# Performance work log

Measured on AMD Instinct MI355X. Metric: run time of the kernel, lower is better.

The kernel has to match this reference:

```python
import jax, jax.numpy as jnp
import numpy as np

N_NODES = 100000
N_EDGES = 800000
N_GRAPHS = 64
D_IN = 128
D_HID = 128
D_OUT = 128
N_VARS = 8


def setup_inputs() -> dict:
    key = jax.random.key(0)
    ks = jax.random.split(key, 12)
    s = 1.0 / np.sqrt(D_IN)
    inp = {
        "features": jax.random.normal(ks[0], (N_NODES, D_IN), jnp.float32),
        "src": jax.random.randint(ks[1], (N_EDGES,), 0, N_NODES, jnp.int32),
        "dst": jax.random.randint(ks[2], (N_EDGES,), 0, N_NODES, jnp.int32),
        "graph_id": jnp.sort(jax.random.randint(ks[3], (N_NODES,), 0, N_GRAPHS, jnp.int32)),
        # GINConv MLP params (Linear + ReLU per layer)
        "W1": jax.random.normal(ks[4], (D_IN, D_HID), jnp.float32) * s,
        "b1": jnp.zeros((D_HID,), jnp.float32),
        "W2": jax.random.normal(ks[5], (D_HID, D_HID), jnp.float32) * s,
        "b2": jnp.zeros((D_HID,), jnp.float32),
        "W3": jax.random.normal(ks[6], (D_HID, D_OUT), jnp.float32) * s,
        "b3": jnp.zeros((D_OUT,), jnp.float32),
        # final prediction head
        "Wp": jax.random.normal(ks[7], (D_OUT, N_VARS), jnp.float32) * s,
        "bp": jnp.zeros((N_VARS,), jnp.float32),
    }
    return inp


def reference(features, src, dst, graph_id, W1, b1, W2, b2, W3, b3, Wp, bp):
    N = features.shape[0]

    def gin_layer(x, W, b):
        # DGL GINConv with eps=0: apply_func(x + sum_{j in N(i)} x_j)
        agg = jax.ops.segment_sum(x[src], dst, num_segments=N)  # [N, d]
        return jax.nn.relu((x + agg) @ W + b)

    h = gin_layer(features, W1, b1)  # dropout p=0 -> identity
    h = gin_layer(h, W2, b2)
    h = gin_layer(h, W3, b3)

    # dgl.mean_nodes: ragged per-graph mean readout
    sums = jax.ops.segment_sum(h, graph_id, num_segments=N_GRAPHS)          # [G, d]
    cnts = jax.ops.segment_sum(jnp.ones((N, 1), h.dtype), graph_id, num_segments=N_GRAPHS)
    pooled = sums / jnp.maximum(cnts, 1.0)
    return pooled @ Wp + bp  # [G, n_vars]
```

## Files before the change

### kernel.cpp

```cpp
#include <hip/hip_runtime.h>
#include <cstddef>

#define NN 100000
#define NE 800000
#define NG 64
#define DD 128
#define NV 8
#define NS 8
#define SCAN_CH 1024
#define SCAN_NB ((NN + SCAN_CH - 1) / SCAN_CH)
#define NPC 256
#define NCHUNK ((NN + NPC - 1) / NPC)

#define CVT_BLKS 6250
#define WT_BLKS 192
#define HIST_BLKS 3125
#define HCH 392
#define ECH ((NE + HCH - 1) / HCH)
#define RNG 12500

typedef __attribute__((ext_vector_type(8))) short bf16x8;
typedef __attribute__((ext_vector_type(4))) float f32x4;
typedef __attribute__((ext_vector_type(2))) unsigned int u32x2;

__device__ inline float lo2f(unsigned int u) {
  union { unsigned int i; float f; } x;
  x.i = u << 16;
  return x.f;
}
__device__ inline float hi2f(unsigned int u) {
  union { unsigned int i; float f; } x;
  x.i = u & 0xffff0000u;
  return x.f;
}
__device__ inline unsigned int pk2(float a, float b) {
  unsigned int r;
  asm("v_cvt_pk_bf16_f32 %0, %1, %2" : "=v"(r) : "v"(a), "v"(b));
  return r;
}
__device__ inline unsigned short f2b(float f) {
  union { float f; unsigned int i; } x;
  x.f = f;
  unsigned int r = x.i + 0x7fffu + ((x.i >> 16) & 1u);
  return (unsigned short)(r >> 16);
}

__global__ __launch_bounds__(256) void prep(const float* __restrict__ feat,
                                            const float* __restrict__ W1,
                                            const float* __restrict__ W2,
                                            const float* __restrict__ W3,
                                            unsigned short* __restrict__ xs,
                                            unsigned short* __restrict__ Wt) {
  int b = blockIdx.x;
  if (b < CVT_BLKS) {
    int tid = b * 256 + threadIdx.x;
    int l = tid & 63, w = tid >> 6;
    int s = w & 7, nb = w >> 3;
    int node = nb * 32 + (l >> 1);
    int half = l & 1;
    const float* p = feat + (size_t)node * DD + s * 16 + half * 8;
    float4 v0 = *(const float4*)p;
    float4 v1 = *(const float4*)(p + 4);
    uint4 o;
    o.x = pk2(v0.x, v0.y);
    o.y = pk2(v0.z, v0.w);
    o.z = pk2(v1.x, v1.y);
    o.w = pk2(v1.z, v1.w);
    *(uint4*)((char*)xs + ((size_t)s * NN + node) * 32 + half * 16) = o;
  } else {
    int idx = (b - CVT_BLKS) * 256 + threadIdx.x;
    int w = idx >> 14, r = idx & 16383;
    const float* W = (w == 0) ? W1 : (w == 1) ? W2 : W3;
    Wt[idx] = f2b(W[(r & 127) * DD + (r >> 7)]);
  }
}

__global__ __launch_bounds__(256) void hist_dst(const int* __restrict__ dst,
                                                int* __restrict__ deg) {
  int e = blockIdx.x * 256 + threadIdx.x;
  if (e < NE) atomicAdd(&deg[dst[e]], 1);
}

__global__ __launch_bounds__(256) void scan1(const int* __restrict__ deg,
                                             int* __restrict__ excl,
                                             int* __restrict__ bsum) {
  __shared__ int ts[256];
  int base = blockIdx.x * SCAN_CH;
  int t = threadIdx.x;
  int v[4];
  int s = 0;
#pragma unroll
  for (int i = 0; i < 4; i++) {
    int idx = base + t * 4 + i;
    v[i] = (idx < NN) ? deg[idx] : 0;
    s += v[i];
  }
  ts[t] = s;
  __syncthreads();
  for (int off = 1; off < 256; off <<= 1) {
    int val = (t >= off) ? ts[t - off] : 0;
    __syncthreads();
    ts[t] += val;
    __syncthreads();
  }
  if (t == 255) bsum[blockIdx.x] = ts[255];
  int run = ts[t] - s;
#pragma unroll
  for (int i = 0; i < 4; i++) {
    int idx = base + t * 4 + i;
    if (idx < NN) excl[idx] = run;
    run += v[i];
  }
}

__global__ __launch_bounds__(128) void scan2(int* __restrict__ bsum, int nb) {
  __shared__ int sh[128];
  int t = threadIdx.x;
  int v = (t < nb) ? bsum[t] : 0;
  sh[t] = v;
  __syncthreads();
  for (int off = 1; off < 128; off <<= 1) {
    int u = (t >= off) ? sh[t - off] : 0;
    __syncthreads();
    sh[t] += u;
    __syncthreads();
  }
  if (t < nb) bsum[t] = sh[t] - v;
}

__global__ __launch_bounds__(256) void scan3(int* __restrict__ rowp,
                                             const int* __restrict__ bsum,
                                             int* __restrict__ cursor) {
  int i = blockIdx.x * blockDim.x + threadIdx.x;
  if (i < NN) {
    int v = rowp[i] + bsum[i / SCAN_CH];
    rowp[i] = v;
    cursor[i] = v;
  }
  if (i == 0) rowp[NN] = NE;
}

__global__ __launch_bounds__(256) void fill_csr(const int* __restrict__ src,
                                                const int* __restrict__ dst,
                                                int* __restrict__ cursor,
                                                int* __restrict__ csrb) {
  int r = blockIdx.x & 7, chunk = blockIdx.x >> 3;
  int lo = r * RNG, hi = lo + RNG;
  int e0 = chunk * ECH;
  int e1 = e0 + ECH;
  if (e1 > NE) e1 = NE;
  for (int e = e0 + threadIdx.x; e < e1; e += 256) {
    int d = dst[e];
    if (d >= lo && d < hi) {
      int pos = atomicAdd(&cursor[d], 1);
      csrb[pos] = src[e] << 5;
    }
  }
}

__global__ __launch_bounds__(256) void gather_slice(const unsigned short* __restrict__ xs,
                                                    const int* __restrict__ csrb,
                                                    const int* __restrict__ rowp,
                                                    unsigned short* __restrict__ aggs) {
  const int s = blockIdx.x & 7;
  const int chunk = blockIdx.x >> 3;
  const char* __restrict__ xsl = (const char*)xs + (size_t)s * NN * 32;
  char* __restrict__ asl = (char*)aggs + (size_t)s * NN * 32;
  const int li = threadIdx.x & 3;
  const int grp = threadIdx.x >> 2;
  const int node0 = chunk * NPC;
  int node1 = node0 + NPC;
  if (node1 > NN) node1 = NN;
  const int lo8 = li * 8;
  for (int n = node0 + grp; n < node1; n += 64) {
    int beg = rowp[n], end = rowp[n + 1];
    u32x2 sv = *(const u32x2*)(xsl + (size_t)n * 32 + lo8);
    float a0 = lo2f(sv.x), a1 = hi2f(sv.x), a2 = lo2f(sv.y), a3 = hi2f(sv.y);
    float c0 = 0.f, c1 = 0.f, c2 = 0.f, c3 = 0.f;
    int e = beg;
    int off = (beg < end) ? csrb[(beg + li < end) ? beg + li : end - 1] : 0;
    for (; e + 4 <= end; e += 4) {
      int ne = e + 4;
      int off_next = 0;
      if (ne < end) off_next = csrb[(ne + li < end) ? ne + li : end - 1];
      int o0 = __shfl(off, 0, 4);
      int o1 = __shfl(off, 1, 4);
      int o2 = __shfl(off, 2, 4);
      int o3 = __shfl(off, 3, 4);
      u32x2 v0 = *(const u32x2*)(xsl + (unsigned int)o0 + lo8);
      u32x2 v1 = *(const u32x2*)(xsl + (unsigned int)o1 + lo8);
      u32x2 v2 = *(const u32x2*)(xsl + (unsigned int)o2 + lo8);
      u32x2 v3 = *(const u32x2*)(xsl + (unsigned int)o3 + lo8);
      a0 += lo2f(v0.x); a1 += hi2f(v0.x); a2 += lo2f(v0.y); a3 += hi2f(v0.y);
      c0 += lo2f(v1.x); c1 += hi2f(v1.x); c2 += lo2f(v1.y); c3 += hi2f(v1.y);
      a0 += lo2f(v2.x); a1 += hi2f(v2.x); a2 += lo2f(v2.y); a3 += hi2f(v2.y);
      c0 += lo2f(v3.x); c1 += hi2f(v3.x); c2 += lo2f(v3.y); c3 += hi2f(v3.y);
      off = off_next;
    }
    if (e < end) {
      int rem = end - e;
      for (int j = 0; j < rem; j++) {
        int oj = __shfl(off, j, 4);
        u32x2 v = *(const u32x2*)(xsl + (unsigned int)oj + lo8);
        a0 += lo2f(v.x); a1 += hi2f(v.x); a2 += lo2f(v.y); a3 += hi2f(v.y);
      }
    }
    u32x2 o;
    o.x = pk2(a0 + c0, a1 + c1);
    o.y = pk2(a2 + c2, a3 + c3);
    *(u32x2*)(asl + (size_t)n * 32 + lo8) = o;
  }
}

template <int POOL>
__global__ __launch_bounds__(256) void gemm_mfma(const unsigned short* __restrict__ A,
                                                 const unsigned short* __restrict__ Wt,
                                                 const float* __restrict__ bias,
                                                 unsigned short* __restrict__ H,
                                                 const int* __restrict__ gid,
                                                 float* __restrict__ sums,
                                                 float* __restrict__ cnts) {
  __shared__ uint4 a_sh4[1024];
  __shared__ uint4 w_sh4[2048];
  __shared__ int gsh[64];
  char* a_sh = (char*)a_sh4;
  char* w_sh = (char*)w_sh4;
  const int t = threadIdx.x;
  const int block_row = blockIdx.x * 64;

  if (POOL) {
    if (t < 64) gsh[t] = (block_row + t < NN) ? gid[block_row + t] : -1;
  }

#pragma unroll
  for (int p = 0; p < 8; p++) {
    int lin = p * 4096 + t * 16;
    int row = lin >> 8, inner = lin & 255;
    uint4 v = *(const uint4*)((const char*)Wt + lin);
    *(uint4*)(w_sh + row * 256 + (inner ^ ((row & 7) << 4))) = v;
  }
#pragma unroll
  for (int p = 0; p < 4; p++) {
    int lin = p * 4096 + t * 16;
    int row = lin >> 8, inner = lin & 255;
    int grow = block_row + row;
    uint4 v = make_uint4(0u, 0u, 0u, 0u);
    if (grow < NN) {
      int slice = inner >> 5, half = (inner >> 4) & 1;
      v = *(const uint4*)((const char*)A + ((size_t)slice * NN + grow) * 32 + half * 16);
    }
    *(uint4*)(a_sh + row * 256 + (inner ^ ((row & 7) << 4))) = v;
  }
  __syncthreads();

  const int wid = t >> 6, lane = t & 63;
  const int rowbase = wid * 16;
  const int lr = lane & 15, lk = lane >> 4;

  f32x4 acc[8];
#pragma unroll
  for (int i = 0; i < 8; i++) acc[i] = (f32x4){0.f, 0.f, 0.f, 0.f};

#pragma unroll
  for (int c = 0; c < 4; c++) {
    int arow = rowbase + lr;
    bf16x8 af = *(const bf16x8*)(a_sh + arow * 256 + ((c * 64 + lk * 16) ^ ((arow & 7) << 4)));
#pragma unroll
    for (int nt = 0; nt < 8; nt++) {
      int bcol = nt * 16 + lr;
      bf16x8 bf = *(const bf16x8*)(w_sh + bcol * 256 + ((c * 64 + lk * 16) ^ ((bcol & 7) << 4)));
      acc[nt] = __builtin_amdgcn_mfma_f32_16x16x32_bf16(af, bf, acc[nt], 0, 0, 0);
    }
  }
  __syncthreads();

  float* osh = (float*)w_sh;
#pragma unroll
  for (int nt = 0; nt < 8; nt++) {
    int col = nt * 16 + lr;
    float bv = bias[col];
#pragma unroll
    for (int r = 0; r < 4; r++) {
      int row = rowbase + lk * 4 + r;
      osh[row * 128 + col] = fmaxf(acc[nt][r] + bv, 0.f);
    }
  }
  __syncthreads();

  if (POOL == 0) {
#pragma unroll
    for (int i = 0; i < 8; i++) {
      int fidx = i * 1024 + t * 4;
      float4 v = *(const float4*)(osh + fidx);
      int row = fidx >> 7, col = fidx & 127;
      int grow = block_row + row;
      if (grow < NN) {
        int slice = col >> 4, w = col & 15;
        u32x2 o;
        o.x = pk2(v.x, v.y);
        o.y = pk2(v.z, v.w);
        *(u32x2*)(H + ((size_t)slice * NN + grow) * 16 + w) = o;
      }
    }
  } else {
    if (t < 128) {
      int f = t;
      float acc2 = 0.f;
      int cnt = 0;
      int cur = gsh[0];
      for (int r = 0; r < 64; r++) {
        int g = gsh[r];
        if (g < 0) break;
        if (g != cur) {
          unsafeAtomicAdd(&sums[cur * DD + f], acc2);
          if (f == 0) unsafeAtomicAdd(&cnts[cur], (float)cnt);
          acc2 = 0.f;
          cnt = 0;
          cur = g;
        }
        acc2 += osh[r * 128 + f];
        cnt++;
      }
      if (cur >= 0 && cnt > 0) {
        unsafeAtomicAdd(&sums[cur * DD + f], acc2);
        if (f == 0) unsafeAtomicAdd(&cnts[cur], (float)cnt);
      }
    }
  }
}

__global__ __launch_bounds__(512) void head(const float* __restrict__ sums,
                                            const float* __restrict__ cnts,
                                            const float* __restrict__ Wp,
                                            const float* __restrict__ bp,
                                            float* __restrict__ out) {
  int t = threadIdx.x;
  int g = t >> 3;
  int v = t & 7;
  float cnt = cnts[g];
  if (cnt < 1.f) cnt = 1.f;
  float acc = 0.f;
  for (int d = 0; d < DD; d++) acc += sums[g * DD + d] * Wp[d * NV + v];
  out[t] = acc / cnt + bp[v];
}

extern "C" void kernel_launch(void* const* d_in, const int* in_sizes, int n_in,
                              void* d_out, int out_size, void* d_ws, size_t ws_size,
                              hipStream_t stream) {
  const float* feat = (const float*)d_in[0];
  const int* src = (const int*)d_in[1];
  const int* dst = (const int*)d_in[2];
  const int* gid = (const int*)d_in[3];
  const float* W1 = (const float*)d_in[4];
  const float* b1 = (const float*)d_in[5];
  const float* W2 = (const float*)d_in[6];
  const float* b2 = (const float*)d_in[7];
  const float* W3 = (const float*)d_in[8];
  const float* b3 = (const float*)d_in[9];
  const float* Wp = (const float*)d_in[10];
  const float* bp = (const float*)d_in[11];
  float* out = (float*)d_out;

  char* ws = (char*)d_ws;
  const size_t matb = (size_t)NN * DD;
  unsigned short* xs0 = (unsigned short*)ws;
  unsigned short* hs = xs0 + matb;
  unsigned short* aggs = hs + matb;
  unsigned short* wtb = aggs + matb;
  float* sums = (float*)(wtb + 3 * DD * DD);
  float* cnts = sums + NG * DD;
  int* deg = (int*)(cnts + NG);
  int* rowp = deg + NN;
  int* cursor = rowp + NN + 1;
  int* bsum = cursor + NN;
  int* csrb = bsum + 128;

  const int nzero = NG * DD + NG + NN;
  hipMemsetAsync(sums, 0, (size_t)nzero * 4, stream);

  prep<<<CVT_BLKS + WT_BLKS, 256, 0, stream>>>(feat, W1, W2, W3, xs0, wtb);
  hist_dst<<<HIST_BLKS, 256, 0, stream>>>(dst, deg);

  scan1<<<SCAN_NB, 256, 0, stream>>>(deg, rowp, bsum);
  scan2<<<1, 128, 0, stream>>>(bsum, SCAN_NB);
  scan3<<<(NN + 255) / 256, 256, 0, stream>>>(rowp, bsum, cursor);
  fill_csr<<<8 * HCH, 256, 0, stream>>>(src, dst, cursor, csrb);

  const int ggrid = NCHUNK * NS;
  const int mgrid = (NN + 63) / 64;
  gather_slice<<<ggrid, 256, 0, stream>>>(xs0, csrb, rowp, aggs);
  gemm_mfma<0><<<mgrid, 256, 0, stream>>>(aggs, wtb, b1, hs, nullptr, nullptr, nullptr);
  gather_slice<<<ggrid, 256, 0, stream>>>(hs, csrb, rowp, aggs);
  gemm_mfma<0><<<mgrid, 256, 0, stream>>>(aggs, wtb + DD * DD, b2, xs0, nullptr, nullptr, nullptr);
  gather_slice<<<ggrid, 256, 0, stream>>>(xs0, csrb, rowp, aggs);
  gemm_mfma<1><<<mgrid, 256, 0, stream>>>(aggs, wtb + 2 * DD * DD, b3, nullptr, gid, sums, cnts);

  head<<<1, 512, 0, stream>>>(sums, cnts, Wp, bp, out);
}
```

Measured before the change: 308.0 us.

## Widen feature slices from 32B to 64B per node in gather layout

Changes the sliced bf16 feature layout from 8 slices of 16 features (32B rows) to 4 slices of 32 features (64B rows). The gather kernel now uses 8 lanes per node and unrolls 8 edges per step, and each block handles half a chunk for one slice. Prep, fill_csr offset shift, gemm load and gemm store are updated to match. The aim is fewer, wider random gathers per edge with better cache-line use, at the cost of a larger per-slice working set in cache.

```diff
diff --git a/kernel.cpp b/kernel.cpp
--- a/kernel.cpp
+++ b/kernel.cpp
@@ -6,7 +6,6 @@
 #define NG 64
 #define DD 128
 #define NV 8
-#define NS 8
 #define SCAN_CH 1024
 #define SCAN_NB ((NN + SCAN_CH - 1) / SCAN_CH)
 #define NPC 256
@@ -54,11 +53,8 @@
   int b = blockIdx.x;
   if (b < CVT_BLKS) {
     int tid = b * 256 + threadIdx.x;
-    int l = tid & 63, w = tid >> 6;
-    int s = w & 7, nb = w >> 3;
-    int node = nb * 32 + (l >> 1);
-    int half = l & 1;
-    const float* p = feat + (size_t)node * DD + s * 16 + half * 8;
+    int n = tid >> 4, part = tid & 15;
+    const float* p = feat + (size_t)n * DD + part * 8;
     float4 v0 = *(const float4*)p;
     float4 v1 = *(const float4*)(p + 4);
     uint4 o;
@@ -66,7 +62,8 @@
     o.y = pk2(v0.z, v0.w);
     o.z = pk2(v1.x, v1.y);
     o.w = pk2(v1.z, v1.w);
-    *(uint4*)((char*)xs + ((size_t)s * NN + node) * 32 + half * 16) = o;
+    int s2 = part >> 2, sub = part & 3;
+    *(uint4*)((char*)xs + ((size_t)s2 * NN + n) * 64 + sub * 16) = o;
   } else {
     int idx = (b - CVT_BLKS) * 256 + threadIdx.x;
     int w = idx >> 14, r = idx & 16383;
@@ -153,7 +150,7 @@
     int d = dst[e];
     if (d >= lo && d < hi) {
       int pos = atomicAdd(&cursor[d], 1);
-      csrb[pos] = src[e] << 5;
+      csrb[pos] = src[e] << 6;
     }
   }
 }
@@ -162,45 +159,58 @@
                                                     const int* __restrict__ csrb,
                                                     const int* __restrict__ rowp,
                                                     unsigned short* __restrict__ aggs) {
-  const int s = blockIdx.x & 7;
+  const int q = blockIdx.x & 7;
+  const int s2 = q & 3, half = q >> 2;
   const int chunk = blockIdx.x >> 3;
-  const char* __restrict__ xsl = (const char*)xs + (size_t)s * NN * 32;
-  char* __restrict__ asl = (char*)aggs + (size_t)s * NN * 32;
-  const int li = threadIdx.x & 3;
-  const int grp = threadIdx.x >> 2;
-  const int node0 = chunk * NPC;
-  int node1 = node0 + NPC;
+  const char* __restrict__ xsl = (const char*)xs + (size_t)s2 * NN * 64;
+  char* __restrict__ asl = (char*)aggs + (size_t)s2 * NN * 64;
+  const int li = threadIdx.x & 7;
+  const int grp = threadIdx.x >> 3;
+  int node0 = chunk * NPC + half * (NPC / 2);
+  int node1 = node0 + NPC / 2;
   if (node1 > NN) node1 = NN;
   const int lo8 = li * 8;
-  for (int n = node0 + grp; n < node1; n += 64) {
+  for (int n = node0 + grp; n < node1; n += 32) {
     int beg = rowp[n], end = rowp[n + 1];
-    u32x2 sv = *(const u32x2*)(xsl + (size_t)n * 32 + lo8);
+    u32x2 sv = *(const u32x2*)(xsl + (size_t)n * 64 + lo8);
     float a0 = lo2f(sv.x), a1 = hi2f(sv.x), a2 = lo2f(sv.y), a3 = hi2f(sv.y);
     float c0 = 0.f, c1 = 0.f, c2 = 0.f, c3 = 0.f;
     int e = beg;
     int off = (beg < end) ? csrb[(beg + li < end) ? beg + li : end - 1] : 0;
-    for (; e + 4 <= end; e += 4) {
-      int ne = e + 4;
+    for (; e + 8 <= end; e += 8) {
+      int ne = e + 8;
       int off_next = 0;
       if (ne < end) off_next = csrb[(ne + li < end) ? ne + li : end - 1];
-      int o0 = __shfl(off, 0, 4);
-      int o1 = __shfl(off, 1, 4);
-      int o2 = __shfl(off, 2, 4);
-      int o3 = __shfl(off, 3, 4);
+      int o0 = __shfl(off, 0, 8);
+      int o1 = __shfl(off, 1, 8);
+      int o2 = __shfl(off, 2, 8);
+      int o3 = __shfl(off, 3, 8);
+      int o4 = __shfl(off, 4, 8);
+      int o5 = __shfl(off, 5, 8);
+      int o6 = __shfl(off, 6, 8);
+      int o7 = __shfl(off, 7, 8);
       u32x2 v0 = *(const u32x2*)(xsl + (unsigned int)o0 + lo8);
       u32x2 v1 = *(const u32x2*)(xsl + (unsigned int)o1 + lo8);
       u32x2 v2 = *(const u32x2*)(xsl + (unsigned int)o2 + lo8);
       u32x2 v3 = *(const u32x2*)(xsl + (unsigned int)o3 + lo8);
+      u32x2 v4 = *(const u32x2*)(xsl + (unsigned int)o4 + lo8);
+      u32x2 v5 = *(const u32x2*)(xsl + (unsigned int)o5 + lo8);
+      u32x2 v6 = *(const u32x2*)(xsl + (unsigned int)o6 + lo8);
+      u32x2 v7 = *(const u32x2*)(xsl + (unsigned int)o7 + lo8);
       a0 += lo2f(v0.x); a1 += hi2f(v0.x); a2 += lo2f(v0.y); a3 += hi2f(v0.y);
       c0 += lo2f(v1.x); c1 += hi2f(v1.x); c2 += lo2f(v1.y); c3 += hi2f(v1.y);
       a0 += lo2f(v2.x); a1 += hi2f(v2.x); a2 += lo2f(v2.y); a3 += hi2f(v2.y);
       c0 += lo2f(v3.x); c1 += hi2f(v3.x); c2 += lo2f(v3.y); c3 += hi2f(v3.y);
+      a0 += lo2f(v4.x); a1 += hi2f(v4.x); a2 += lo2f(v4.y); a3 += hi2f(v4.y);
+      c0 += lo2f(v5.x); c1 += hi2f(v5.x); c2 += lo2f(v5.y); c3 += hi2f(v5.y);
+      a0 += lo2f(v6.x); a1 += hi2f(v6.x); a2 += lo2f(v6.y); a3 += hi2f(v6.y);
+      c0 += lo2f(v7.x); c1 += hi2f(v7.x); c2 += lo2f(v7.y); c3 += hi2f(v7.y);
       off = off_next;
     }
     if (e < end) {
       int rem = end - e;
       for (int j = 0; j < rem; j++) {
-        int oj = __shfl(off, j, 4);
+        int oj = __shfl(off, j, 8);
         u32x2 v = *(const u32x2*)(xsl + (unsigned int)oj + lo8);
         a0 += lo2f(v.x); a1 += hi2f(v.x); a2 += lo2f(v.y); a3 += hi2f(v.y);
       }
@@ -208,7 +218,7 @@
     u32x2 o;
     o.x = pk2(a0 + c0, a1 + c1);
     o.y = pk2(a2 + c2, a3 + c3);
-    *(u32x2*)(asl + (size_t)n * 32 + lo8) = o;
+    *(u32x2*)(asl + (size_t)n * 64 + lo8) = o;
   }
 }
 
@@ -246,8 +256,8 @@
     int grow = block_row + row;
     uint4 v = make_uint4(0u, 0u, 0u, 0u);
     if (grow < NN) {
-      int slice = inner >> 5, half = (inner >> 4) & 1;
-      v = *(const uint4*)((const char*)A + ((size_t)slice * NN + grow) * 32 + half * 16);
+      int s2 = inner >> 6, sub = inner & 63;
+      v = *(const uint4*)((const char*)A + ((size_t)s2 * NN + grow) * 64 + sub);
     }
     *(uint4*)(a_sh + row * 256 + (inner ^ ((row & 7) << 4))) = v;
   }
@@ -295,11 +305,11 @@
       int row = fidx >> 7, col = fidx & 127;
       int grow = block_row + row;
       if (grow < NN) {
-        int slice = col >> 4, w = col & 15;
+        int s2 = col >> 5, w = col & 31;
         u32x2 o;
         o.x = pk2(v.x, v.y);
         o.y = pk2(v.z, v.w);
-        *(u32x2*)(H + ((size_t)slice * NN + grow) * 16 + w) = o;
+        *(u32x2*)(H + ((size_t)s2 * NN + grow) * 32 + w) = o;
       }
     }
   } else {
@@ -386,7 +396,7 @@
   scan3<<<(NN + 255) / 256, 256, 0, stream>>>(rowp, bsum, cursor);
   fill_csr<<<8 * HCH, 256, 0, stream>>>(src, dst, cursor, csrb);
 
-  const int ggrid = NCHUNK * NS;
+  const int ggrid = NCHUNK * 8;
   const int mgrid = (NN + 63) / 64;
   gather_slice<<<ggrid, 256, 0, stream>>>(xs0, csrb, rowp, aggs);
   gemm_mfma<0><<<mgrid, 256, 0, stream>>>(aggs, wtb, b1, hs, nullptr, nullptr, nullptr);
```

New measurement: 304.7 us (median of 2 runs). About the same (-1.1%).
